# Kernel tuning notes

Hardware: AMD Instinct MI355X
Metric: run time of the kernel (lower is better)

The kernel has to match this reference:

```python
import jax, jax.numpy as jnp
import numpy as np

NSEG = 65  # instance ids live in [0, NSEG); must match setup_inputs fill_max
EPS = 1e-8


def setup_inputs() -> dict:
    key = jax.random.key(0)
    k1, k2 = jax.random.split(key)
    B, C, H, W = 8, 4, 1024, 1024
    logit = jax.random.normal(k1, (B, C, H, W), dtype=jnp.float32)
    inst_gt = jax.random.randint(k2, (B, H, W), 0, NSEG, dtype=jnp.int32)
    return {"logit": logit, "inst_gt": inst_gt}


def reference(logit, inst_gt):
    B, C, H, W = logit.shape
    N = H * W
    # softmax over channel dim (as F.softmax(logit, dim=1))
    p = jax.nn.softmax(logit, axis=1)                      # [B, C, H, W]
    p = p.reshape(B, C, N).transpose(0, 2, 1).reshape(B * N, C)  # [B*N, C]
    # one fused segment reduce over all batches: offset ids per batch element
    seg = (inst_gt.reshape(B, N) + jnp.arange(B, dtype=inst_gt.dtype)[:, None] * NSEG).reshape(-1)
    sums = jax.ops.segment_sum(p, seg, num_segments=B * NSEG)        # [B*NSEG, C]
    sumsq = jax.ops.segment_sum(p * p, seg, num_segments=B * NSEG)   # [B*NSEG, C]
    cnt = jax.ops.segment_sum(jnp.ones((B * N,), p.dtype), seg, num_segments=B * NSEG)  # [B*NSEG]
    cnt = cnt[:, None]                                               # [B*NSEG, 1]
    # unbiased variance per (batch, instance, channel): (sumsq - sum^2/n) / (n-1)
    n_safe = jnp.where(cnt > 0, cnt, 1.0)
    denom = jnp.where(cnt > 1, cnt - 1.0, 1.0)
    var = (sumsq - sums * sums / n_safe) / denom                     # [B*NSEG, C]
    var = var.reshape(B, NSEG, C)
    cnt = cnt.reshape(B, NSEG, 1)
    nonzero_id = (jnp.arange(NSEG) != 0)[None, :, None]              # skip background id 0
    # only instances with more than 1 pixel contribute variance
    valid = nonzero_id & (cnt > 1.0)
    sum_var = jnp.sum(jnp.where(valid, var, 0.0), axis=(1, 2))       # [B]
    # len(inst_ids): number of distinct nonzero ids present in each image
    num_ids = jnp.sum(jnp.where(nonzero_id[..., 0] & (cnt[..., 0] > 0.0), 1.0, 0.0), axis=1)  # [B]
    loss = jnp.mean(sum_var / (num_ids + EPS))
    return loss
```

## Files before the change

### kernel.cpp

```cpp
#include <hip/hip_runtime.h>


typedef unsigned short u16x2 __attribute__((ext_vector_type(2)));
typedef unsigned int   u32x4 __attribute__((ext_vector_type(4)));
typedef short          s16x8 __attribute__((ext_vector_type(8)));
typedef float          f32x4 __attribute__((ext_vector_type(4)));

constexpr int   B_    = 8;
constexpr int   SEGS  = 64;
constexpr int   VALS  = 5;
constexpr float EPS_  = 1e-8f;

constexpr int PLANE   = 528;
constexpr int NSLOT   = 9;
constexpr int WLDS    = NSLOT * PLANE;
constexpr int LDS_SZ  = (4 * WLDS > 16384) ? 4 * WLDS : 16384;

__device__ __forceinline__ unsigned asu(float f)  { return __float_as_uint(f); }
__device__ __forceinline__ float    asf(unsigned u){ return __uint_as_float(u); }

__global__ __launch_bounds__(256) void vl_accum(const float* __restrict__ logit,
                                                const int*   __restrict__ inst,
                                                float* __restrict__ acc,
                                                int N, int ppb)
{
    __shared__ __align__(16) unsigned char lds[LDS_SZ];

    const int tid  = threadIdx.x;
    const int wid  = tid >> 6;
    const int lane = tid & 63;
    const int col  = lane & 15;
    const int quad = lane >> 4;
    const int wbase = wid * WLDS;

    const bool selLds = (col < 4) | (col >= 8 && col < 12);
    const unsigned cword = (col == 4) ? 0x3F803F80u : 0u;
    const int pl = (col < 4) ? (2 * col)
                 : ((col >= 8 && col < 12) ? (2 * (col - 8) + 1) : 0);
    const int bRd   = wbase + pl * PLANE + quad * 16;
    const int segRd = wbase + 8 * PLANE + quad * 16;
    const int segWr = wbase + 8 * PLANE + lane * 8;

    u16x2 rowdup[4];
#pragma unroll
    for (int t = 0; t < 4; ++t) {
        unsigned short rw = (unsigned short)(t * 16 + col);
        rowdup[t] = (u16x2){rw, rw};
    }
    const u16x2 one2  = (u16x2){1, 1};
    const u16x2 bf1p  = (u16x2){0x3F80, 0x3F80};

    const int b = blockIdx.y;
    const float* __restrict__ l0 = logit + (size_t)b * 4 * N;
    const int*   __restrict__ ib = inst  + (size_t)b * N;

    f32x4 acc0 = {0.f,0.f,0.f,0.f}, acc1 = {0.f,0.f,0.f,0.f};
    f32x4 acc2 = {0.f,0.f,0.f,0.f}, acc3 = {0.f,0.f,0.f,0.f};

    const int blockStart = blockIdx.x * ppb;
    const int rounds = ppb >> 10;
    const int base0  = blockStart + (wid << 8) + (lane << 2);

#define LOAD_ROUND(R, X0, X1, X2, X3, SG)                                       \
    {                                                                           \
        const int q  = base0 + ((R) << 10);                                     \
        const bool ok = (q + 4 <= N);                                           \
        const int qc = ok ? q : 0;                                              \
        X0 = *(const float4*)(l0 + qc);                                         \
        X1 = *(const float4*)(l0 + (size_t)N     + qc);                         \
        X2 = *(const float4*)(l0 + (size_t)2 * N + qc);                         \
        X3 = *(const float4*)(l0 + (size_t)3 * N + qc);                         \
        int4 sgt = *(const int4*)(ib + qc);                                     \
        SG = ok ? sgt : make_int4(0, 0, 0, 0);                                  \
    }

    float4 cx0, cx1, cx2, cx3; int4 csg;
    if (rounds > 0) LOAD_ROUND(0, cx0, cx1, cx2, cx3, csg)

    for (int r = 0; r < rounds; ++r) {
        float4 nx0, nx1, nx2, nx3; int4 nsg;
        if (r + 1 < rounds) LOAD_ROUND(r + 1, nx0, nx1, nx2, nx3, nsg)

        const float c0[4] = {cx0.x, cx0.y, cx0.z, cx0.w};
        const float c1[4] = {cx1.x, cx1.y, cx1.z, cx1.w};
        const float c2[4] = {cx2.x, cx2.y, cx2.z, cx2.w};
        const float c3[4] = {cx3.x, cx3.y, cx3.z, cx3.w};

        float P0[4], P1[4], P2[4], QQ[4];
#pragma unroll
        for (int i = 0; i < 4; ++i) {
            float va = c0[i], vb = c1[i], vc = c2[i], vd = c3[i];
            float m  = fmaxf(fmaxf(va, vb), fmaxf(vc, vd));
            float e0 = __expf(va - m);
            float e1 = __expf(vb - m);
            float e2 = __expf(vc - m);
            float e3 = __expf(vd - m);
            float rr = 1.0f / (e0 + e1 + e2 + e3);
            float q0 = e0 * rr, q1 = e1 * rr, q2 = e2 * rr, q3 = e3 * rr;
            P0[i] = q0; P1[i] = q1; P2[i] = q2;
            QQ[i] = q0*q0 + q1*q1 + q2*q2 + q3*q3;
        }

#define STAGE_PLANE(P, ARR)                                                     \
        {                                                                       \
            unsigned a0 = asu(ARR[0]), a1 = asu(ARR[1]);                        \
            unsigned a2 = asu(ARR[2]), a3 = asu(ARR[3]);                        \
            unsigned h1m = a1 & 0xFFFF0000u, h3m = a3 & 0xFFFF0000u;            \
            unsigned hi01 = (a0 >> 16) | h1m;                                   \
            unsigned hi23 = (a2 >> 16) | h3m;                                   \
            float l0f = ARR[0] - asf(a0 & 0xFFFF0000u);                         \
            float l1f = ARR[1] - asf(h1m);                                      \
            float l2f = ARR[2] - asf(a2 & 0xFFFF0000u);                         \
            float l3f = ARR[3] - asf(h3m);                                      \
            unsigned lo01 = (asu(l0f) >> 16) | (asu(l1f) & 0xFFFF0000u);        \
            unsigned lo23 = (asu(l2f) >> 16) | (asu(l3f) & 0xFFFF0000u);        \
            *(uint2*)(lds + wbase + (2*(P)) * PLANE + lane * 8)   = make_uint2(hi01, hi23); \
            *(uint2*)(lds + wbase + (2*(P)+1) * PLANE + lane * 8) = make_uint2(lo01, lo23); \
        }
        STAGE_PLANE(0, P0)
        STAGE_PLANE(1, P1)
        STAGE_PLANE(2, P2)
        STAGE_PLANE(3, QQ)
#undef STAGE_PLANE

        {
            unsigned r0 = (unsigned)(csg.x - 1) & 0xFFFFu;
            unsigned r1 = (unsigned)(csg.y - 1) & 0xFFFFu;
            unsigned r2 = (unsigned)(csg.z - 1) & 0xFFFFu;
            unsigned r3 = (unsigned)(csg.w - 1) & 0xFFFFu;
            *(uint2*)(lds + segWr) = make_uint2(r0 | (r1 << 16), r2 | (r3 << 16));
        }

#pragma unroll
        for (int kt = 0; kt < 8; ++kt) {
            s16x8 braw = *(const s16x8*)(lds + bRd   + kt * 64);
            u32x4 sv   = *(const u32x4*)(lds + segRd + kt * 64);
            u32x4 bw   = __builtin_bit_cast(u32x4, braw);
#pragma unroll
            for (int i = 0; i < 4; ++i) bw[i] = selLds ? bw[i] : cword;
            s16x8 bfrag = __builtin_bit_cast(s16x8, bw);

#define DO_TILE(T, ACC)                                                         \
            {                                                                   \
                u32x4 fr;                                                       \
                _Pragma("unroll")                                               \
                for (int i = 0; i < 4; ++i) {                                   \
                    u16x2 sp  = __builtin_bit_cast(u16x2, sv[i]);               \
                    u16x2 d   = sp - rowdup[T];                                 \
                    u16x2 mn  = __builtin_elementwise_min(d, one2);             \
                    u16x2 inv = one2 - mn;                                      \
                    u16x2 f   = inv * bf1p;                                     \
                    fr[i] = __builtin_bit_cast(unsigned, f);                    \
                }                                                               \
                s16x8 afrag = __builtin_bit_cast(s16x8, fr);                    \
                ACC = __builtin_amdgcn_mfma_f32_16x16x32_bf16(afrag, bfrag, ACC, 0, 0, 0); \
            }
            DO_TILE(0, acc0)
            DO_TILE(1, acc1)
            DO_TILE(2, acc2)
            DO_TILE(3, acc3)
#undef DO_TILE
        }

        cx0 = nx0; cx1 = nx1; cx2 = nx2; cx3 = nx3; csg = nsg;
    }
#undef LOAD_ROUND

    __syncthreads();
    float* cl = (float*)lds;
    {
        const int base = ((wid * 4) * 64 + lane) * 4;
        *(f32x4*)(cl + base)            = acc0;
        *(f32x4*)(cl + base + 64 * 4)   = acc1;
        *(f32x4*)(cl + base + 128 * 4)  = acc2;
        *(f32x4*)(cl + base + 192 * 4)  = acc3;
    }
    __syncthreads();

    for (int i = tid; i < SEGS * VALS; i += 256) {
        const int row = i / VALS;
        const int cc  = i - row * VALS;
        const int t   = row >> 4;
        const int rr  = row & 15;
        const int g   = rr >> 2;
        const int reg = rr & 3;
        const int lhi = g * 16 + cc;
        const int llo = lhi + 8;
        float v = 0.0f;
#pragma unroll
        for (int w = 0; w < 4; ++w) {
            v += cl[((w * 4 + t) * 64 + lhi) * 4 + reg];
            v += cl[((w * 4 + t) * 64 + llo) * 4 + reg];
        }
        unsafeAtomicAdd(acc + ((size_t)blockIdx.y * SEGS + row) * VALS + cc, v);
    }
}

__global__ __launch_bounds__(256) void vl_finalize(const float* __restrict__ acc,
                                                   float* __restrict__ out)
{
    __shared__ float sum_var[B_];
    __shared__ float num_ids[B_];
    if (threadIdx.x < B_) { sum_var[threadIdx.x] = 0.0f; num_ids[threadIdx.x] = 0.0f; }
    __syncthreads();

    for (int i = threadIdx.x; i < B_ * SEGS; i += 256) {
        const float* a = acc + (size_t)i * VALS;
        const int b = i >> 6;
        const float cnt = a[4];
        if (cnt > 1.0f) {
            const float inv_n = 1.0f / cnt;
            const float denom = cnt - 1.0f;
            const float s0 = a[0], s1 = a[1], s2 = a[2];
            const float s3 = cnt - s0 - s1 - s2;
            const float ssum2 = s0*s0 + s1*s1 + s2*s2 + s3*s3;
            const float sv = (a[3] - ssum2 * inv_n) / denom;
            atomicAdd(&sum_var[b], sv);
        }
        if (cnt > 0.0f) atomicAdd(&num_ids[b], 1.0f);
    }
    __syncthreads();

    if (threadIdx.x == 0) {
        float loss = 0.0f;
#pragma unroll
        for (int b = 0; b < B_; ++b) loss += sum_var[b] / (num_ids[b] + EPS_);
        out[0] = loss / (float)B_;
    }
}

extern "C" void kernel_launch(void* const* d_in, const int* in_sizes, int n_in,
                              void* d_out, int out_size, void* d_ws, size_t ws_size,
                              hipStream_t stream) {
    const float* logit = (const float*)d_in[0];
    const int*   inst  = (const int*)d_in[1];
    float* out = (float*)d_out;
    float* acc = (float*)d_ws;

    const int totalPix = in_sizes[1];
    const int N = totalPix / B_;

    hipMemsetAsync(acc, 0, (size_t)B_ * SEGS * VALS * sizeof(float), stream);

    const int gridx = 256;
    int ppb = (N + gridx - 1) / gridx;
    ppb = (ppb + 1023) & ~1023;

    dim3 grid(gridx, B_);
    vl_accum<<<grid, 256, 0, stream>>>(logit, inst, acc, N, ppb);
    vl_finalize<<<1, 256, 0, stream>>>(acc, out);
}
```

Baseline: 221.6 us.

## Double-buffer LDS staging and split MFMA accumulators to overlap softmax with MFMA

Each wave's LDS staging area is now double-buffered. The softmax and bf16 split staging for the next round run after the current round's MFMA loop and write the alternate buffer, with a sched_barrier separating the loads from the compute. The accumulators are split into even and odd kt chains to shorten MFMA dependency chains, the one-hot construction becomes a single multiply-add, and the grid is halved to 128 blocks per batch with launch_bounds occupancy 4. This raises LDS use per block and gives fewer, longer blocks, which may reduce memory-level parallelism.

```diff
diff --git a/kernel.cpp b/kernel.cpp
--- a/kernel.cpp
+++ b/kernel.cpp
@@ -13,16 +13,17 @@
 
 constexpr int PLANE   = 528;
 constexpr int NSLOT   = 9;
-constexpr int WLDS    = NSLOT * PLANE;
+constexpr int BUFSZ   = NSLOT * PLANE;
+constexpr int WLDS    = 2 * BUFSZ;
 constexpr int LDS_SZ  = (4 * WLDS > 16384) ? 4 * WLDS : 16384;
 
 __device__ __forceinline__ unsigned asu(float f)  { return __float_as_uint(f); }
 __device__ __forceinline__ float    asf(unsigned u){ return __uint_as_float(u); }
 
-__global__ __launch_bounds__(256) void vl_accum(const float* __restrict__ logit,
-                                                const int*   __restrict__ inst,
-                                                float* __restrict__ acc,
-                                                int N, int ppb)
+__global__ __launch_bounds__(256, 4) void vl_accum(const float* __restrict__ logit,
+                                                   const int*   __restrict__ inst,
+                                                   float* __restrict__ accOut,
+                                                   int N, int ppb)
 {
     __shared__ __align__(16) unsigned char lds[LDS_SZ];
 
@@ -37,9 +38,9 @@
     const unsigned cword = (col == 4) ? 0x3F803F80u : 0u;
     const int pl = (col < 4) ? (2 * col)
                  : ((col >= 8 && col < 12) ? (2 * (col - 8) + 1) : 0);
-    const int bRd   = wbase + pl * PLANE + quad * 16;
-    const int segRd = wbase + 8 * PLANE + quad * 16;
-    const int segWr = wbase + 8 * PLANE + lane * 8;
+    const int bRd0   = wbase + pl * PLANE + quad * 16;
+    const int segRd0 = wbase + 8 * PLANE + quad * 16;
+    const int segWr0 = wbase + 8 * PLANE + lane * 8;
 
     u16x2 rowdup[4];
 #pragma unroll
@@ -48,14 +49,15 @@
         rowdup[t] = (u16x2){rw, rw};
     }
     const u16x2 one2  = (u16x2){1, 1};
-    const u16x2 bf1p  = (u16x2){0x3F80, 0x3F80};
+    const u16x2 negb  = (u16x2){0xC080, 0xC080};
+    const u16x2 posb  = (u16x2){0x3F80, 0x3F80};
 
     const int b = blockIdx.y;
     const float* __restrict__ l0 = logit + (size_t)b * 4 * N;
     const int*   __restrict__ ib = inst  + (size_t)b * N;
 
-    f32x4 acc0 = {0.f,0.f,0.f,0.f}, acc1 = {0.f,0.f,0.f,0.f};
-    f32x4 acc2 = {0.f,0.f,0.f,0.f}, acc3 = {0.f,0.f,0.f,0.f};
+    f32x4 acc0a = {0,0,0,0}, acc1a = {0,0,0,0}, acc2a = {0,0,0,0}, acc3a = {0,0,0,0};
+    f32x4 acc0b = {0,0,0,0}, acc1b = {0,0,0,0}, acc2b = {0,0,0,0}, acc3b = {0,0,0,0};
 
     const int blockStart = blockIdx.x * ppb;
     const int rounds = ppb >> 10;
@@ -74,67 +76,76 @@
         SG = ok ? sgt : make_int4(0, 0, 0, 0);                                  \
     }
 
-    float4 cx0, cx1, cx2, cx3; int4 csg;
-    if (rounds > 0) LOAD_ROUND(0, cx0, cx1, cx2, cx3, csg)
+#define SOFTMAX4(X0, X1, X2, X3, P0, P1, P2, QQ)                                \
+    {                                                                           \
+        const float sc0[4] = {X0.x, X0.y, X0.z, X0.w};                          \
+        const float sc1[4] = {X1.x, X1.y, X1.z, X1.w};                          \
+        const float sc2[4] = {X2.x, X2.y, X2.z, X2.w};                          \
+        const float sc3[4] = {X3.x, X3.y, X3.z, X3.w};                          \
+        _Pragma("unroll")                                                       \
+        for (int i = 0; i < 4; ++i) {                                           \
+            float va = sc0[i], vb = sc1[i], vc = sc2[i], vd = sc3[i];           \
+            float m  = fmaxf(fmaxf(va, vb), fmaxf(vc, vd));                     \
+            float e0 = __expf(va - m);                                          \
+            float e1 = __expf(vb - m);                                          \
+            float e2 = __expf(vc - m);                                          \
+            float e3 = __expf(vd - m);                                          \
+            float rr = 1.0f / (e0 + e1 + e2 + e3);                              \
+            float q0 = e0 * rr, q1 = e1 * rr, q2 = e2 * rr, q3 = e3 * rr;       \
+            P0[i] = q0; P1[i] = q1; P2[i] = q2;                                 \
+            QQ[i] = q0*q0 + q1*q1 + q2*q2 + q3*q3;                              \
+        }                                                                       \
+    }
+
+#define STAGE_PLANE(BOFF, P, ARR)                                               \
+    {                                                                           \
+        unsigned a0 = asu(ARR[0]), a1 = asu(ARR[1]);                            \
+        unsigned a2 = asu(ARR[2]), a3 = asu(ARR[3]);                            \
+        unsigned h1m = a1 & 0xFFFF0000u, h3m = a3 & 0xFFFF0000u;                \
+        unsigned hi01 = (a0 >> 16) | h1m;                                       \
+        unsigned hi23 = (a2 >> 16) | h3m;                                       \
+        float l0f = ARR[0] - asf(a0 & 0xFFFF0000u);                             \
+        float l1f = ARR[1] - asf(h1m);                                          \
+        float l2f = ARR[2] - asf(a2 & 0xFFFF0000u);                             \
+        float l3f = ARR[3] - asf(h3m);                                          \
+        unsigned lo01 = (asu(l0f) >> 16) | (asu(l1f) & 0xFFFF0000u);            \
+        unsigned lo23 = (asu(l2f) >> 16) | (asu(l3f) & 0xFFFF0000u);            \
+        *(uint2*)(lds + (BOFF) + wbase + (2*(P)) * PLANE + lane * 8)   = make_uint2(hi01, hi23); \
+        *(uint2*)(lds + (BOFF) + wbase + (2*(P)+1) * PLANE + lane * 8) = make_uint2(lo01, lo23); \
+    }
+
+#define STAGE_ALL(BOFF, P0, P1, P2, QQ, SG)                                     \
+    {                                                                           \
+        STAGE_PLANE(BOFF, 0, P0)                                                \
+        STAGE_PLANE(BOFF, 1, P1)                                                \
+        STAGE_PLANE(BOFF, 2, P2)                                                \
+        STAGE_PLANE(BOFF, 3, QQ)                                                \
+        unsigned r0 = (unsigned)(SG.x - 1) & 0xFFFFu;                           \
+        unsigned r1 = (unsigned)(SG.y - 1) & 0xFFFFu;                           \
+        unsigned r2 = (unsigned)(SG.z - 1) & 0xFFFFu;                           \
+        unsigned r3 = (unsigned)(SG.w - 1) & 0xFFFFu;                           \
+        *(uint2*)(lds + (BOFF) + segWr0) = make_uint2(r0 | (r1 << 16), r2 | (r3 << 16)); \
+    }
+
+    if (rounds > 0) {
+        float4 cx0, cx1, cx2, cx3; int4 csg;
+        LOAD_ROUND(0, cx0, cx1, cx2, cx3, csg)
+        float P0[4], P1[4], P2[4], QQ[4];
+        SOFTMAX4(cx0, cx1, cx2, cx3, P0, P1, P2, QQ)
+        STAGE_ALL(0, P0, P1, P2, QQ, csg)
+    }
 
     for (int r = 0; r < rounds; ++r) {
         float4 nx0, nx1, nx2, nx3; int4 nsg;
-        if (r + 1 < rounds) LOAD_ROUND(r + 1, nx0, nx1, nx2, nx3, nsg)
-
-        const float c0[4] = {cx0.x, cx0.y, cx0.z, cx0.w};
-        const float c1[4] = {cx1.x, cx1.y, cx1.z, cx1.w};
-        const float c2[4] = {cx2.x, cx2.y, cx2.z, cx2.w};
-        const float c3[4] = {cx3.x, cx3.y, cx3.z, cx3.w};
-
-        float P0[4], P1[4], P2[4], QQ[4];
-#pragma unroll
-        for (int i = 0; i < 4; ++i) {
-            float va = c0[i], vb = c1[i], vc = c2[i], vd = c3[i];
-            float m  = fmaxf(fmaxf(va, vb), fmaxf(vc, vd));
-            float e0 = __expf(va - m);
-            float e1 = __expf(vb - m);
-            float e2 = __expf(vc - m);
-            float e3 = __expf(vd - m);
-            float rr = 1.0f / (e0 + e1 + e2 + e3);
-            float q0 = e0 * rr, q1 = e1 * rr, q2 = e2 * rr, q3 = e3 * rr;
-            P0[i] = q0; P1[i] = q1; P2[i] = q2;
-            QQ[i] = q0*q0 + q1*q1 + q2*q2 + q3*q3;
-        }
-
-#define STAGE_PLANE(P, ARR)                                                     \
-        {                                                                       \
-            unsigned a0 = asu(ARR[0]), a1 = asu(ARR[1]);                        \
-            unsigned a2 = asu(ARR[2]), a3 = asu(ARR[3]);                        \
-            unsigned h1m = a1 & 0xFFFF0000u, h3m = a3 & 0xFFFF0000u;            \
-            unsigned hi01 = (a0 >> 16) | h1m;                                   \
-            unsigned hi23 = (a2 >> 16) | h3m;                                   \
-            float l0f = ARR[0] - asf(a0 & 0xFFFF0000u);                         \
-            float l1f = ARR[1] - asf(h1m);                                      \
-            float l2f = ARR[2] - asf(a2 & 0xFFFF0000u);                         \
-            float l3f = ARR[3] - asf(h3m);                                      \
-            unsigned lo01 = (asu(l0f) >> 16) | (asu(l1f) & 0xFFFF0000u);        \
-            unsigned lo23 = (asu(l2f) >> 16) | (asu(l3f) & 0xFFFF0000u);        \
-            *(uint2*)(lds + wbase + (2*(P)) * PLANE + lane * 8)   = make_uint2(hi01, hi23); \
-            *(uint2*)(lds + wbase + (2*(P)+1) * PLANE + lane * 8) = make_uint2(lo01, lo23); \
-        }
-        STAGE_PLANE(0, P0)
-        STAGE_PLANE(1, P1)
-        STAGE_PLANE(2, P2)
-        STAGE_PLANE(3, QQ)
-#undef STAGE_PLANE
-
-        {
-            unsigned r0 = (unsigned)(csg.x - 1) & 0xFFFFu;
-            unsigned r1 = (unsigned)(csg.y - 1) & 0xFFFFu;
-            unsigned r2 = (unsigned)(csg.z - 1) & 0xFFFFu;
-            unsigned r3 = (unsigned)(csg.w - 1) & 0xFFFFu;
-            *(uint2*)(lds + segWr) = make_uint2(r0 | (r1 << 16), r2 | (r3 << 16));
-        }
-
+        const bool hasNext = (r + 1 < rounds);
+        if (hasNext) LOAD_ROUND(r + 1, nx0, nx1, nx2, nx3, nsg)
+        __builtin_amdgcn_sched_barrier(0);
+
+        const int bufOff = (r & 1) * BUFSZ;
 #pragma unroll
         for (int kt = 0; kt < 8; ++kt) {
-            s16x8 braw = *(const s16x8*)(lds + bRd   + kt * 64);
-            u32x4 sv   = *(const u32x4*)(lds + segRd + kt * 64);
+            s16x8 braw = *(const s16x8*)(lds + bufOff + bRd0   + kt * 64);
+            u32x4 sv   = *(const u32x4*)(lds + bufOff + segRd0 + kt * 64);
             u32x4 bw   = __builtin_bit_cast(u32x4, braw);
 #pragma unroll
             for (int i = 0; i < 4; ++i) bw[i] = selLds ? bw[i] : cword;
@@ -148,23 +159,36 @@
                     u16x2 sp  = __builtin_bit_cast(u16x2, sv[i]);               \
                     u16x2 d   = sp - rowdup[T];                                 \
                     u16x2 mn  = __builtin_elementwise_min(d, one2);             \
-                    u16x2 inv = one2 - mn;                                      \
-                    u16x2 f   = inv * bf1p;                                     \
+                    u16x2 f   = mn * negb + posb;              \
                     fr[i] = __builtin_bit_cast(unsigned, f);                    \
                 }                                                               \
                 s16x8 afrag = __builtin_bit_cast(s16x8, fr);                    \
                 ACC = __builtin_amdgcn_mfma_f32_16x16x32_bf16(afrag, bfrag, ACC, 0, 0, 0); \
             }
-            DO_TILE(0, acc0)
-            DO_TILE(1, acc1)
-            DO_TILE(2, acc2)
-            DO_TILE(3, acc3)
+            if ((kt & 1) == 0) {
+                DO_TILE(0, acc0a) DO_TILE(1, acc1a) DO_TILE(2, acc2a) DO_TILE(3, acc3a)
+            } else {
+                DO_TILE(0, acc0b) DO_TILE(1, acc1b) DO_TILE(2, acc2b) DO_TILE(3, acc3b)
+            }
 #undef DO_TILE
         }
 
-        cx0 = nx0; cx1 = nx1; cx2 = nx2; cx3 = nx3; csg = nsg;
+        if (hasNext) {
+            float P0[4], P1[4], P2[4], QQ[4];
+            SOFTMAX4(nx0, nx1, nx2, nx3, P0, P1, P2, QQ)
+            const int nOff = ((r + 1) & 1) * BUFSZ;
+            STAGE_ALL(nOff, P0, P1, P2, QQ, nsg)
+        }
     }
 #undef LOAD_ROUND
+#undef SOFTMAX4
+#undef STAGE_PLANE
+#undef STAGE_ALL
+
+    f32x4 acc0 = acc0a + acc0b;
+    f32x4 acc1 = acc1a + acc1b;
+    f32x4 acc2 = acc2a + acc2b;
+    f32x4 acc3 = acc3a + acc3b;
 
     __syncthreads();
     float* cl = (float*)lds;
@@ -192,7 +216,7 @@
             v += cl[((w * 4 + t) * 64 + lhi) * 4 + reg];
             v += cl[((w * 4 + t) * 64 + llo) * 4 + reg];
         }
-        unsafeAtomicAdd(acc + ((size_t)blockIdx.y * SEGS + row) * VALS + cc, v);
+        unsafeAtomicAdd(accOut + ((size_t)blockIdx.y * SEGS + row) * VALS + cc, v);
     }
 }
 
@@ -242,7 +266,7 @@
 
     hipMemsetAsync(acc, 0, (size_t)B_ * SEGS * VALS * sizeof(float), stream);
 
-    const int gridx = 256;
+    const int gridx = 128;
     int ppb = (N + gridx - 1) / gridx;
     ppb = (ppb + 1023) & ~1023;
 
```

Result: no change. 219.3 us (median of 2 runs) (-1.0%).
